# Kernel tuning notes

Hardware: AMD Instinct MI355X
Metric: run time of the kernel (lower is better)

The kernel has to match this reference:

```python
import jax, jax.numpy as jnp
import numpy as np

FEATURE_DIM = 256
TEMP = 0.1
BASE_TEMP = 0.07
MAX_SAMPLES = 1024
SIM_THR = 0.7


def setup_inputs() -> dict:
    key = jax.random.key(0)
    ks = jax.random.split(key, 8)
    B, C, H, W = 4, FEATURE_DIM, 160, 160
    s = 1.0 / np.sqrt(C)
    return {
        'feats': jax.random.normal(ks[0], (B, C, H, W), jnp.float32),
        'labels': jax.random.randint(ks[1], (B, H, W), 0, 2).astype(jnp.int64),
        'superpixel_indice': jax.random.randint(ks[2], (B, H, W), 0, 200).astype(jnp.int64),
        'w1': jax.random.normal(ks[3], (C, C), jnp.float32) * s,
        'b1': jnp.zeros((C,), jnp.float32),
        'w2': jax.random.normal(ks[4], (C, C), jnp.float32) * s,
        'b2': jnp.zeros((C,), jnp.float32),
        'wa1': jax.random.normal(ks[5], (64, C), jnp.float32) * s,
        'ba1': jnp.zeros((64,), jnp.float32),
        'wa2': jax.random.normal(ks[6], (1, 64), jnp.float32) * (1.0 / 8.0),
        'ba2': jnp.zeros((1,), jnp.float32),
    }


def _per_sample(f, w, lab, sp):
    # f: (N, C) normalized proj feats, w: (N,) pixel weights, lab/sp: (N,) int
    valid = lab == 1
    # deterministic sample: stable-sort valid pixels to the front, take MAX_SAMPLES
    order = jnp.argsort(jnp.where(valid, 0, 1).astype(jnp.int32))
    idx = order[:MAX_SAMPLES]
    sel = valid[idx]                       # (S,) real-sample mask (pads if <S valid)
    tf = f[idx]                            # (S, C)
    tw = w[idx]                            # (S,)
    ts = sp[idx]                           # (S,)
    sim = tf @ tf.T                        # (S, S)
    S = MAX_SAMPLES
    eye = jnp.eye(S, dtype=bool)
    pos = (ts[:, None] == ts[None, :]) & (sim > SIM_THR)
    pos = pos & sel[:, None] & sel[None, :] & ~eye
    exp_sim = jnp.exp(sim / TEMP) * sel[None, :].astype(sim.dtype)
    denom = exp_sim.sum(axis=1)            # (S,)
    log_prob = sim / TEMP - jnp.log(jnp.where(denom > 0, denom, 1.0))[:, None]
    pw = tw[:, None] * tw[None, :]
    pwm = jnp.where(pos, pw, 0.0)
    psum = pwm.sum()
    loss = -(TEMP / BASE_TEMP) * (pwm * jnp.where(pos, log_prob, 0.0)).sum() / jnp.where(psum > 0, psum, 1.0)
    has = psum > 0
    return jnp.where(has, loss, 0.0), has


def reference(feats, labels, superpixel_indice, w1, b1, w2, b2, wa1, ba1, wa2, ba2):
    B, C, H, W = feats.shape
    x = jnp.transpose(feats, (0, 2, 3, 1)).reshape(B, H * W, C)  # (B, N, C)
    proj = jax.nn.relu(x @ w1.T + b1) @ w2.T + b2                # 1x1 convs == per-pixel matmul
    attn = jax.nn.sigmoid(jax.nn.relu(x @ wa1.T + ba1) @ wa2.T + ba2)[..., 0]  # (B, N)
    nrm = jnp.linalg.norm(proj, axis=-1, keepdims=True)
    fn = proj / jnp.maximum(nrm, 1e-12)
    lab = labels.reshape(B, -1)
    sp = superpixel_indice.reshape(B, -1)
    losses, flags = jax.vmap(_per_sample)(fn, attn, lab, sp)
    n = flags.sum().astype(jnp.float32)
    return jnp.where(n > 0, losses.sum() / jnp.maximum(n, 1.0), 0.0)
```

## Files before the change

### kernel.cpp

```cpp
#include <hip/hip_runtime.h>
#include <hip/hip_bf16.h>
#include <math.h>

#define NPIX   25600
#define CDIM   256
#define SSEL   1024
#define BATCH  4
#define NCHUNK 25
#define INV_T  10.0f
#define RATIO  1.4285714285714286f
#define THR    0.7f

typedef __attribute__((ext_vector_type(8))) short bf16x8;
typedef __attribute__((ext_vector_type(4))) float f32x4;
typedef unsigned short u16;

__device__ __forceinline__ u16 to_bf16(float v) {
  __hip_bfloat16 h = __float2bfloat16(v);
  return *reinterpret_cast<u16*>(&h);
}

__global__ __launch_bounds__(256) void pack_weights(
    const float* __restrict__ w1, const float* __restrict__ w2,
    const float* __restrict__ wa1, const int* __restrict__ labels,
    u16* __restrict__ w1b, u16* __restrict__ w2b, u16* __restrict__ wab,
    float* __restrict__ denom, float* __restrict__ Prow, float* __restrict__ Ssum,
    int* __restrict__ counts) {
  int t = threadIdx.x;
  int e = blockIdx.x * 256 + t;
  if (e < 65536) {
    w1b[e] = to_bf16(w1[e]);
    w2b[e] = to_bf16(w2[e]);
  }
  if (e < 16384) wab[e] = to_bf16(wa1[e]);
  if (e < BATCH * SSEL) { denom[e] = 0.f; Prow[e] = 0.f; }
  if (e < BATCH) Ssum[e] = 0.f;

  if (blockIdx.x < BATCH * NCHUNK) {
    int b = blockIdx.x / NCHUNK, ch = blockIdx.x % NCHUNK;
    const int* lab = labels + b * NPIX + ch * 1024;
    int local = 0;
#pragma unroll
    for (int qq = 0; qq < 4; ++qq) local += (lab[qq * 256 + t] == 1);
    for (int off = 32; off > 0; off >>= 1) local += __shfl_xor(local, off, 64);
    __shared__ int ws[4];
    if ((t & 63) == 0) ws[t >> 6] = local;
    __syncthreads();
    if (t == 0) counts[blockIdx.x] = ws[0] + ws[1] + ws[2] + ws[3];
  }
}

__global__ __launch_bounds__(1024) void select_scatter(
    const int* __restrict__ labels, const int* __restrict__ sp,
    const int* __restrict__ counts,
    int* __restrict__ idx, int* __restrict__ selv, int* __restrict__ tsp) {
  int b = blockIdx.x / NCHUNK, ch = blockIdx.x % NCHUNK;
  int t = threadIdx.x;
  __shared__ int cs[NCHUNK];
  __shared__ int wave_tot[16];
  if (t < NCHUNK) cs[t] = counts[b * NCHUNK + t];
  __syncthreads();
  int Vtot = 0, vbase = 0;
#pragma unroll
  for (int c = 0; c < NCHUNK; ++c) {
    int v = cs[c];
    Vtot += v;
    if (c < ch) vbase += v;
  }
  int ibase = ch * 1024 - vbase;

  int i = ch * 1024 + t;
  int isv = (labels[b * NPIX + i] == 1) ? 1 : 0;
  int lane = t & 63, wid = t >> 6;
  unsigned long long mv = __ballot(isv);
  int pv = __popcll(mv & ((1ull << lane) - 1ull));
  if (lane == 0) wave_tot[wid] = __popcll(mv);
  __syncthreads();
  for (int w = 0; w < wid; ++w) pv += wave_tot[w];
  int gslot = isv ? (vbase + pv) : (Vtot + ibase + (t - pv));
  if (gslot < SSEL) {
    idx [b * SSEL + gslot] = i;
    selv[b * SSEL + gslot] = isv;
    tsp [b * SSEL + gslot] = sp[b * NPIX + i];
  }
}

__global__ __launch_bounds__(256) void gather_cast(
    const float* __restrict__ feats, const int* __restrict__ idx,
    u16* __restrict__ xh) {
  int r0 = blockIdx.x * 16;
  int b  = r0 >> 10;
  int t  = threadIdx.x;
  __shared__ int ridx[16];
  if (t < 16) ridx[t] = idx[r0 + t];
  __syncthreads();
  const float* fb = feats + ((long)b * CDIM + t) * NPIX;
#pragma unroll 4
  for (int r = 0; r < 16; ++r) {
    xh[(long)(r0 + r) * CDIM + t] = to_bf16(fb[ridx[r]]);
  }
}

__global__ __launch_bounds__(256) void gemm1_kernel(
    const u16* __restrict__ xh, const u16* __restrict__ w1b,
    const u16* __restrict__ wab,
    const float* __restrict__ b1, const float* __restrict__ ba1,
    const float* __restrict__ wa2, const float* __restrict__ ba2,
    u16* __restrict__ hh, float* __restrict__ tw) {
  int n  = blockIdx.x;
  int i0 = blockIdx.y * 64;
  int t = threadIdx.x;
  int lane = t & 63, w = t >> 6, m = lane & 15, q = lane >> 4;
  bool attn = (n == 4);
  const u16* bsrc = attn ? wab : (w1b + n * 64 * 256);

  __shared__ __align__(16) u16 Ah[64 * 72];
  __shared__ __align__(16) u16 Bh[64 * 72];

  f32x4 acc[4];
#pragma unroll
  for (int nt = 0; nt < 4; ++nt) acc[nt] = {0.f, 0.f, 0.f, 0.f};

  for (int kk = 0; kk < 4; ++kk) {
    __syncthreads();
#pragma unroll
    for (int p = 0; p < 2; ++p) {
      int e = p * 256 + t;
      int row = e >> 3, kg = e & 7;
      int lo = row * 72 + kg * 8;
      *(uint4*)&Ah[lo] = *(const uint4*)&xh[(i0 + row) * 256 + kk * 64 + kg * 8];
      *(uint4*)&Bh[lo] = *(const uint4*)&bsrc[row * 256 + kk * 64 + kg * 8];
    }
    __syncthreads();
#pragma unroll
    for (int ks = 0; ks < 2; ++ks) {
      int koff = ks * 32 + q * 8;
      bf16x8 ah = *(const bf16x8*)&Ah[(w * 16 + m) * 72 + koff];
#pragma unroll
      for (int nt = 0; nt < 4; ++nt) {
        bf16x8 bh = *(const bf16x8*)&Bh[(nt * 16 + m) * 72 + koff];
        acc[nt] = __builtin_amdgcn_mfma_f32_16x16x32_bf16(ah, bh, acc[nt], 0, 0, 0);
      }
    }
  }

  if (!attn) {
#pragma unroll
    for (int nt = 0; nt < 4; ++nt) {
      int col = n * 64 + nt * 16 + m;
      float bb = b1[col];
#pragma unroll
      for (int reg = 0; reg < 4; ++reg) {
        int row = i0 + w * 16 + q * 4 + reg;
        hh[row * 256 + col] = to_bf16(fmaxf(acc[nt][reg] + bb, 0.f));
      }
    }
  } else {
    float part[4] = {0.f, 0.f, 0.f, 0.f};
#pragma unroll
    for (int nt = 0; nt < 4; ++nt) {
      int ca = nt * 16 + m;
      float bb = ba1[ca], wv = wa2[ca];
#pragma unroll
      for (int reg = 0; reg < 4; ++reg)
        part[reg] += fmaxf(acc[nt][reg] + bb, 0.f) * wv;
    }
    for (int off = 8; off > 0; off >>= 1) {
#pragma unroll
      for (int reg = 0; reg < 4; ++reg)
        part[reg] += __shfl_xor(part[reg], off, 64);
    }
    if (m == 0) {
      float bb2 = ba2[0];
#pragma unroll
      for (int reg = 0; reg < 4; ++reg) {
        int row = i0 + w * 16 + q * 4 + reg;
        tw[row] = 1.f / (1.f + expf(-(part[reg] + bb2)));
      }
    }
  }
}

__global__ __launch_bounds__(256) void gemm2norm_kernel(
    const u16* __restrict__ hh, const u16* __restrict__ w2b,
    const float* __restrict__ b2, u16* __restrict__ fnb) {
  int i0 = blockIdx.x * 64;
  int t = threadIdx.x;
  int lane = t & 63, w = t >> 6, m = lane & 15, q = lane >> 4;

  __shared__ __align__(16) u16 Bs[64 * 264];

  bf16x8 af[8];
#pragma unroll
  for (int ks = 0; ks < 8; ++ks)
    af[ks] = *(const bf16x8*)&hh[(i0 + w * 16 + m) * 256 + ks * 32 + q * 8];

  f32x4 acc[4][4];
#pragma unroll
  for (int n = 0; n < 4; ++n)
#pragma unroll
    for (int nt = 0; nt < 4; ++nt) acc[n][nt] = {0.f, 0.f, 0.f, 0.f};

  for (int n = 0; n < 4; ++n) {
    __syncthreads();
#pragma unroll
    for (int i = 0; i < 8; ++i) {
      int e = i * 256 + t;
      int row = e >> 5, kg = e & 31;
      *(uint4*)&Bs[row * 264 + kg * 8] = *(const uint4*)&w2b[(n * 64 + row) * 256 + kg * 8];
    }
    __syncthreads();
#pragma unroll
    for (int ks = 0; ks < 8; ++ks) {
      int koff = ks * 32 + q * 8;
#pragma unroll
      for (int nt = 0; nt < 4; ++nt) {
        bf16x8 bh = *(const bf16x8*)&Bs[(nt * 16 + m) * 264 + koff];
        acc[n][nt] = __builtin_amdgcn_mfma_f32_16x16x32_bf16(af[ks], bh, acc[n][nt], 0, 0, 0);
      }
    }
  }

  float ss[4] = {0.f, 0.f, 0.f, 0.f};
#pragma unroll
  for (int n = 0; n < 4; ++n)
#pragma unroll
    for (int nt = 0; nt < 4; ++nt) {
      float bb = b2[n * 64 + nt * 16 + m];
#pragma unroll
      for (int reg = 0; reg < 4; ++reg) {
        float p = acc[n][nt][reg] + bb;
        acc[n][nt][reg] = p;
        ss[reg] += p * p;
      }
    }
  for (int off = 8; off > 0; off >>= 1) {
#pragma unroll
    for (int reg = 0; reg < 4; ++reg) ss[reg] += __shfl_xor(ss[reg], off, 64);
  }
  float inv[4];
#pragma unroll
  for (int reg = 0; reg < 4; ++reg)
    inv[reg] = 1.f / fmaxf(sqrtf(ss[reg]), 1e-12f);

#pragma unroll
  for (int n = 0; n < 4; ++n)
#pragma unroll
    for (int nt = 0; nt < 4; ++nt) {
      int col = n * 64 + nt * 16 + m;
#pragma unroll
      for (int reg = 0; reg < 4; ++reg) {
        int row = i0 + w * 16 + q * 4 + reg;
        fnb[row * 256 + col] = to_bf16(acc[n][nt][reg] * inv[reg]);
      }
    }
}

__global__ __launch_bounds__(256) void sim_kernel(
    const u16* __restrict__ fnb, const float* __restrict__ tw,
    const int* __restrict__ selv, const int* __restrict__ tsp,
    float* __restrict__ denom, float* __restrict__ Prow, float* __restrict__ Ssum) {
  int b = blockIdx.y;
  int t = threadIdx.x;
  int lane = t & 63, w = t >> 6;
  int m = lane & 15, q = lane >> 4;

  int rem = blockIdx.x, ti = 0;
  while (rem >= (16 - ti)) { rem -= (16 - ti); ++ti; }
  int tj = ti + rem;
  bool diag = (ti == tj);
  int i0 = ti * 64, j0 = tj * 64;
  int base = b << 10;

  __shared__ __align__(16) u16 Ah[64 * 72];
  __shared__ __align__(16) u16 Bhh[64 * 72];
  __shared__ float drl[64], Prl[64];
  __shared__ float dclw[4][64], Pclw[4][64];
  __shared__ float swv[4];

  const u16* Bh = diag ? Ah : Bhh;

  f32x4 acc[4];
#pragma unroll
  for (int nt = 0; nt < 4; ++nt) acc[nt] = {0.f, 0.f, 0.f, 0.f};

  for (int kk = 0; kk < 4; ++kk) {
    __syncthreads();
#pragma unroll
    for (int p = 0; p < 2; ++p) {
      int e = p * 256 + t;
      int row = e >> 3, kg = e & 7;
      int lo = row * 72 + kg * 8;
      *(uint4*)&Ah[lo] = *(const uint4*)&fnb[(base + i0 + row) * 256 + kk * 64 + kg * 8];
      if (!diag)
        *(uint4*)&Bhh[lo] = *(const uint4*)&fnb[(base + j0 + row) * 256 + kk * 64 + kg * 8];
    }
    __syncthreads();
#pragma unroll
    for (int ks = 0; ks < 2; ++ks) {
      int koff = ks * 32 + q * 8;
      bf16x8 ah = *(const bf16x8*)&Ah[(w * 16 + m) * 72 + koff];
#pragma unroll
      for (int nt = 0; nt < 4; ++nt) {
        bf16x8 bh = *(const bf16x8*)&Bh[(nt * 16 + m) * 72 + koff];
        acc[nt] = __builtin_amdgcn_mfma_f32_16x16x32_bf16(ah, bh, acc[nt], 0, 0, 0);
      }
    }
  }

  int   gi[4], gj[4], si[4], sj[4], ci[4], cj[4];
  float twi[4], twj[4];
#pragma unroll
  for (int reg = 0; reg < 4; ++reg) {
    int i = i0 + w * 16 + q * 4 + reg;
    gi[reg] = i; twi[reg] = tw[base + i];
    si[reg] = selv[base + i]; ci[reg] = tsp[base + i];
  }
#pragma unroll
  for (int nt = 0; nt < 4; ++nt) {
    int j = j0 + nt * 16 + m;
    gj[nt] = j; twj[nt] = tw[base + j];
    sj[nt] = selv[base + j]; cj[nt] = tsp[base + j];
  }

  float dR[4] = {0, 0, 0, 0}, PR[4] = {0, 0, 0, 0};
  float dC[4] = {0, 0, 0, 0}, PC[4] = {0, 0, 0, 0};
  float Sp = 0.f;
#pragma unroll
  for (int nt = 0; nt < 4; ++nt) {
#pragma unroll
    for (int reg = 0; reg < 4; ++reg) {
      float s = acc[nt][reg];
      float e10 = __expf(s * INV_T);
      if (sj[nt]) dR[reg] += e10;
      if (si[reg]) dC[nt] += e10;
      if (si[reg] && sj[nt] && (ci[reg] == cj[nt]) && (s > THR) && (gi[reg] != gj[nt])) {
        float pw = twi[reg] * twj[nt];
        PR[reg] += pw;
        PC[nt] += pw;
        Sp += pw * s;
      }
    }
  }

  for (int off = 8; off > 0; off >>= 1) {
#pragma unroll
    for (int reg = 0; reg < 4; ++reg) {
      dR[reg] += __shfl_xor(dR[reg], off, 64);
      PR[reg] += __shfl_xor(PR[reg], off, 64);
    }
  }
  if (m == 0) {
#pragma unroll
    for (int reg = 0; reg < 4; ++reg) {
      drl[w * 16 + q * 4 + reg] = dR[reg];
      Prl[w * 16 + q * 4 + reg] = PR[reg];
    }
  }
  if (!diag) {
    for (int off = 32; off >= 16; off >>= 1) {
#pragma unroll
      for (int nt = 0; nt < 4; ++nt) {
        dC[nt] += __shfl_xor(dC[nt], off, 64);
        PC[nt] += __shfl_xor(PC[nt], off, 64);
      }
    }
    if (q == 0) {
#pragma unroll
      for (int nt = 0; nt < 4; ++nt) {
        dclw[w][nt * 16 + m] = dC[nt];
        Pclw[w][nt * 16 + m] = PC[nt];
      }
    }
  }
  for (int off = 32; off > 0; off >>= 1) Sp += __shfl_xor(Sp, off, 64);
  if (lane == 0) swv[w] = Sp;
  __syncthreads();

  if (t < 64) {
    atomicAdd(&denom[base + i0 + t], drl[t]);
    atomicAdd(&Prow [base + i0 + t], Prl[t]);
    if (!diag) {
      float dc = dclw[0][t] + dclw[1][t] + dclw[2][t] + dclw[3][t];
      float pc = Pclw[0][t] + Pclw[1][t] + Pclw[2][t] + Pclw[3][t];
      atomicAdd(&denom[base + j0 + t], dc);
      atomicAdd(&Prow [base + j0 + t], pc);
    }
  }
  if (t == 0) {
    float St = swv[0] + swv[1] + swv[2] + swv[3];
    atomicAdd(&Ssum[b], diag ? St : 2.f * St);
  }
}

__global__ __launch_bounds__(1024) void finalize_kernel(
    const float* __restrict__ denom, const float* __restrict__ Prow,
    const float* __restrict__ Ssum, float* __restrict__ out) {
  int t = threadIdx.x;
  int b = t >> 8, u = t & 255;
  float P = 0.f, L = 0.f;
#pragma unroll
  for (int q = 0; q < 4; ++q) {
    int s = u + q * 256;
    float p = Prow[b * SSEL + s];
    float D = denom[b * SSEL + s];
    P += p;
    L += p * logf(D > 0.f ? D : 1.f);
  }
  for (int off = 32; off > 0; off >>= 1) {
    P += __shfl_xor(P, off, 64);
    L += __shfl_xor(L, off, 64);
  }
  __shared__ float wP[16], wL[16];
  int lane = t & 63, w = t >> 6;
  if (lane == 0) { wP[w] = P; wL[w] = L; }
  __syncthreads();
  if (t == 0) {
    float total = 0.f, n = 0.f;
    for (int bb = 0; bb < BATCH; ++bb) {
      float psum = wP[4 * bb] + wP[4 * bb + 1] + wP[4 * bb + 2] + wP[4 * bb + 3];
      float lsum = wL[4 * bb] + wL[4 * bb + 1] + wL[4 * bb + 2] + wL[4 * bb + 3];
      if (psum > 0.f) {
        float wls = Ssum[bb] * INV_T - lsum;
        total += -RATIO * wls / psum;
        n += 1.f;
      }
    }
    out[0] = (n > 0.f) ? (total / n) : 0.f;
  }
}

extern "C" void kernel_launch(void* const* d_in, const int* in_sizes, int n_in,
                              void* d_out, int out_size, void* d_ws, size_t ws_size,
                              hipStream_t stream) {
  const float* feats = (const float*)d_in[0];
  const int*   labels = (const int*)d_in[1];
  const int*   sp     = (const int*)d_in[2];
  const float* w1  = (const float*)d_in[3];
  const float* b1  = (const float*)d_in[4];
  const float* w2  = (const float*)d_in[5];
  const float* b2  = (const float*)d_in[6];
  const float* wa1 = (const float*)d_in[7];
  const float* ba1 = (const float*)d_in[8];
  const float* wa2 = (const float*)d_in[9];
  const float* ba2 = (const float*)d_in[10];
  float* out = (float*)d_out;

  char* W = (char*)d_ws;
  u16* w1b = (u16*)W;               W += 65536 * 2;
  u16* w2b = (u16*)W;               W += 65536 * 2;
  u16* wab = (u16*)W;               W += 16384 * 2;
  u16* xh  = (u16*)W;               W += 1048576 * 2;
  u16* hh  = (u16*)W;               W += 1048576 * 2;
  u16* fnb = (u16*)W;               W += 1048576 * 2;
  float* tw   = (float*)W;          W += 4096 * 4;
  float* denom= (float*)W;          W += 4096 * 4;
  float* Prow = (float*)W;          W += 4096 * 4;
  float* Ssum = (float*)W;          W += 4 * 4;
  int*   idx  = (int*)W;            W += 4096 * 4;
  int*   selv = (int*)W;            W += 4096 * 4;
  int*   tsp  = (int*)W;            W += 4096 * 4;
  int*   counts = (int*)W;          W += 128 * 4;

  pack_weights<<<256, 256, 0, stream>>>(w1, w2, wa1, labels, w1b, w2b, wab,
                                        denom, Prow, Ssum, counts);
  select_scatter<<<BATCH * NCHUNK, 1024, 0, stream>>>(labels, sp, counts,
                                                      idx, selv, tsp);
  gather_cast<<<256, 256, 0, stream>>>(feats, idx, xh);
  gemm1_kernel<<<dim3(5, 64), 256, 0, stream>>>(xh, w1b, wab, b1, ba1,
                                                wa2, ba2, hh, tw);
  gemm2norm_kernel<<<64, 256, 0, stream>>>(hh, w2b, b2, fnb);
  sim_kernel<<<dim3(136, BATCH), 256, 0, stream>>>(fnb, tw, selv, tsp,
                                                   denom, Prow, Ssum);
  finalize_kernel<<<1, 1024, 0, stream>>>(denom, Prow, Ssum, out);
}
```

Before: 197.1 us.

## Fuse pipeline into three kernels: merged prep, fused MLP, sim with last-block finalize

Merges label counting and scatter into one prep kernel, where each block recounts all chunks itself, and folds the weight casts into extra blocks of it. Fuses the gather, first GEMM, attention head, second GEMM and normalisation into one kernel, keeping intermediates in shared memory and reading weights straight from global memory. Finalize moves into the sim kernel through a last-block atomic counter, and the sim tile is loaded in one pass with full K. This cuts seven launches to three and removes the xh/hh round trips through global memory, but the fused MLP runs only 64 blocks and each prep block reads labels 25 times.

```diff
diff --git a/kernel.cpp b/kernel.cpp
--- a/kernel.cpp
+++ b/kernel.cpp
@@ -10,6 +10,7 @@
 #define INV_T  10.0f
 #define RATIO  1.4285714285714286f
 #define THR    0.7f
+#define NBLK_SIM (136 * BATCH)
 
 typedef __attribute__((ext_vector_type(8))) short bf16x8;
 typedef __attribute__((ext_vector_type(4))) float f32x4;
@@ -20,238 +21,202 @@
   return *reinterpret_cast<u16*>(&h);
 }
 
-__global__ __launch_bounds__(256) void pack_weights(
+__global__ __launch_bounds__(1024) void prep_kernel(
     const float* __restrict__ w1, const float* __restrict__ w2,
-    const float* __restrict__ wa1, const int* __restrict__ labels,
+    const float* __restrict__ wa1,
+    const int* __restrict__ labels, const int* __restrict__ sp,
     u16* __restrict__ w1b, u16* __restrict__ w2b, u16* __restrict__ wab,
-    float* __restrict__ denom, float* __restrict__ Prow, float* __restrict__ Ssum,
-    int* __restrict__ counts) {
+    float* __restrict__ denom, float* __restrict__ Prow,
+    float* __restrict__ Ssum, unsigned* __restrict__ donecnt,
+    int* __restrict__ idx, int* __restrict__ selv, int* __restrict__ tsp) {
+  __shared__ int wcnt[NCHUNK][16];
+  __shared__ int cs[NCHUNK];
   int t = threadIdx.x;
-  int e = blockIdx.x * 256 + t;
-  if (e < 65536) {
+  int blk = blockIdx.x;
+
+  if (blk < BATCH * NCHUNK) {
+    int b = blk / NCHUNK, ch = blk % NCHUNK;
+    int lane = t & 63, wid = t >> 6;
+    int my_isv = 0;
+    unsigned long long my_mv = 0;
+    for (int c = 0; c < NCHUNK; ++c) {
+      int isv = (labels[b * NPIX + c * 1024 + t] == 1) ? 1 : 0;
+      unsigned long long mv = __ballot(isv);
+      if (c == ch) { my_isv = isv; my_mv = mv; }
+      if (lane == 0) wcnt[c][wid] = __popcll(mv);
+    }
+    __syncthreads();
+    if (t < NCHUNK) {
+      int s = 0;
+      for (int w = 0; w < 16; ++w) s += wcnt[t][w];
+      cs[t] = s;
+    }
+    __syncthreads();
+    int Vtot = 0, vbase = 0;
+    for (int c = 0; c < NCHUNK; ++c) {
+      int v = cs[c];
+      Vtot += v;
+      if (c < ch) vbase += v;
+    }
+    int ibase = ch * 1024 - vbase;
+    int pv = __popcll(my_mv & ((1ull << lane) - 1ull));
+    for (int w = 0; w < wid; ++w) pv += wcnt[ch][w];
+    int i = ch * 1024 + t;
+    int gslot = my_isv ? (vbase + pv) : (Vtot + ibase + (t - pv));
+    if (gslot < SSEL) {
+      idx [b * SSEL + gslot] = i;
+      selv[b * SSEL + gslot] = my_isv;
+      tsp [b * SSEL + gslot] = sp[b * NPIX + i];
+    }
+  } else {
+    int e = (blk - BATCH * NCHUNK) * 1024 + t;
     w1b[e] = to_bf16(w1[e]);
     w2b[e] = to_bf16(w2[e]);
-  }
-  if (e < 16384) wab[e] = to_bf16(wa1[e]);
-  if (e < BATCH * SSEL) { denom[e] = 0.f; Prow[e] = 0.f; }
-  if (e < BATCH) Ssum[e] = 0.f;
-
-  if (blockIdx.x < BATCH * NCHUNK) {
-    int b = blockIdx.x / NCHUNK, ch = blockIdx.x % NCHUNK;
-    const int* lab = labels + b * NPIX + ch * 1024;
-    int local = 0;
-#pragma unroll
-    for (int qq = 0; qq < 4; ++qq) local += (lab[qq * 256 + t] == 1);
-    for (int off = 32; off > 0; off >>= 1) local += __shfl_xor(local, off, 64);
-    __shared__ int ws[4];
-    if ((t & 63) == 0) ws[t >> 6] = local;
-    __syncthreads();
-    if (t == 0) counts[blockIdx.x] = ws[0] + ws[1] + ws[2] + ws[3];
+    if (e < 16384) wab[e] = to_bf16(wa1[e]);
+    if (e < BATCH * SSEL) { denom[e] = 0.f; Prow[e] = 0.f; }
+    if (e < BATCH) Ssum[e] = 0.f;
+    if (e == 0) *donecnt = 0u;
   }
 }
 
-__global__ __launch_bounds__(1024) void select_scatter(
-    const int* __restrict__ labels, const int* __restrict__ sp,
-    const int* __restrict__ counts,
-    int* __restrict__ idx, int* __restrict__ selv, int* __restrict__ tsp) {
-  int b = blockIdx.x / NCHUNK, ch = blockIdx.x % NCHUNK;
-  int t = threadIdx.x;
-  __shared__ int cs[NCHUNK];
-  __shared__ int wave_tot[16];
-  if (t < NCHUNK) cs[t] = counts[b * NCHUNK + t];
-  __syncthreads();
-  int Vtot = 0, vbase = 0;
-#pragma unroll
-  for (int c = 0; c < NCHUNK; ++c) {
-    int v = cs[c];
-    Vtot += v;
-    if (c < ch) vbase += v;
-  }
-  int ibase = ch * 1024 - vbase;
-
-  int i = ch * 1024 + t;
-  int isv = (labels[b * NPIX + i] == 1) ? 1 : 0;
-  int lane = t & 63, wid = t >> 6;
-  unsigned long long mv = __ballot(isv);
-  int pv = __popcll(mv & ((1ull << lane) - 1ull));
-  if (lane == 0) wave_tot[wid] = __popcll(mv);
-  __syncthreads();
-  for (int w = 0; w < wid; ++w) pv += wave_tot[w];
-  int gslot = isv ? (vbase + pv) : (Vtot + ibase + (t - pv));
-  if (gslot < SSEL) {
-    idx [b * SSEL + gslot] = i;
-    selv[b * SSEL + gslot] = isv;
-    tsp [b * SSEL + gslot] = sp[b * NPIX + i];
-  }
-}
-
-__global__ __launch_bounds__(256) void gather_cast(
+__global__ __launch_bounds__(256) void mlp_fused(
     const float* __restrict__ feats, const int* __restrict__ idx,
-    u16* __restrict__ xh) {
-  int r0 = blockIdx.x * 16;
-  int b  = r0 >> 10;
-  int t  = threadIdx.x;
-  __shared__ int ridx[16];
-  if (t < 16) ridx[t] = idx[r0 + t];
-  __syncthreads();
-  const float* fb = feats + ((long)b * CDIM + t) * NPIX;
-#pragma unroll 4
-  for (int r = 0; r < 16; ++r) {
-    xh[(long)(r0 + r) * CDIM + t] = to_bf16(fb[ridx[r]]);
-  }
-}
-
-__global__ __launch_bounds__(256) void gemm1_kernel(
-    const u16* __restrict__ xh, const u16* __restrict__ w1b,
+    const u16* __restrict__ w1b, const u16* __restrict__ w2b,
     const u16* __restrict__ wab,
     const float* __restrict__ b1, const float* __restrict__ ba1,
     const float* __restrict__ wa2, const float* __restrict__ ba2,
-    u16* __restrict__ hh, float* __restrict__ tw) {
-  int n  = blockIdx.x;
-  int i0 = blockIdx.y * 64;
-  int t = threadIdx.x;
+    const float* __restrict__ b2,
+    u16* __restrict__ fnb, float* __restrict__ tw) {
+  int i0 = blockIdx.x * 64;
+  int b  = i0 >> 10;
+  int t  = threadIdx.x;
   int lane = t & 63, w = t >> 6, m = lane & 15, q = lane >> 4;
-  bool attn = (n == 4);
-  const u16* bsrc = attn ? wab : (w1b + n * 64 * 256);
-
-  __shared__ __align__(16) u16 Ah[64 * 72];
-  __shared__ __align__(16) u16 Bh[64 * 72];
-
-  f32x4 acc[4];
-#pragma unroll
-  for (int nt = 0; nt < 4; ++nt) acc[nt] = {0.f, 0.f, 0.f, 0.f};
-
-  for (int kk = 0; kk < 4; ++kk) {
-    __syncthreads();
-#pragma unroll
-    for (int p = 0; p < 2; ++p) {
-      int e = p * 256 + t;
-      int row = e >> 3, kg = e & 7;
-      int lo = row * 72 + kg * 8;
-      *(uint4*)&Ah[lo] = *(const uint4*)&xh[(i0 + row) * 256 + kk * 64 + kg * 8];
-      *(uint4*)&Bh[lo] = *(const uint4*)&bsrc[row * 256 + kk * 64 + kg * 8];
-    }
-    __syncthreads();
-#pragma unroll
-    for (int ks = 0; ks < 2; ++ks) {
+
+  __shared__ __align__(16) u16 xs[64 * 264];
+  __shared__ __align__(16) u16 hs[64 * 264];
+  __shared__ int ridx[64];
+
+  if (t < 64) ridx[t] = idx[i0 + t];
+  __syncthreads();
+
+  const float* fb = feats + ((long)b * CDIM + t) * NPIX;
+#pragma unroll 8
+  for (int r = 0; r < 64; ++r)
+    xs[r * 264 + t] = to_bf16(fb[ridx[r]]);
+  __syncthreads();
+
+  bf16x8 af[8];
+#pragma unroll
+  for (int ks = 0; ks < 8; ++ks)
+    af[ks] = *(const bf16x8*)&xs[(w * 16 + m) * 264 + ks * 32 + q * 8];
+
+  for (int g = 0; g < 5; ++g) {
+    bool attn = (g == 4);
+    const u16* bsrc = attn ? wab : (w1b + g * 64 * 256);
+    f32x4 acc[4];
+#pragma unroll
+    for (int nt = 0; nt < 4; ++nt) acc[nt] = {0.f, 0.f, 0.f, 0.f};
+#pragma unroll
+    for (int ks = 0; ks < 8; ++ks) {
       int koff = ks * 32 + q * 8;
-      bf16x8 ah = *(const bf16x8*)&Ah[(w * 16 + m) * 72 + koff];
-#pragma unroll
-      for (int nt = 0; nt < 4; ++nt) {
-        bf16x8 bh = *(const bf16x8*)&Bh[(nt * 16 + m) * 72 + koff];
-        acc[nt] = __builtin_amdgcn_mfma_f32_16x16x32_bf16(ah, bh, acc[nt], 0, 0, 0);
-      }
-    }
-  }
-
-  if (!attn) {
+#pragma unroll
+      for (int nt = 0; nt < 4; ++nt) {
+        bf16x8 bh = *(const bf16x8*)&bsrc[(nt * 16 + m) * 256 + koff];
+        acc[nt] = __builtin_amdgcn_mfma_f32_16x16x32_bf16(af[ks], bh, acc[nt], 0, 0, 0);
+      }
+    }
+    if (!attn) {
+#pragma unroll
+      for (int nt = 0; nt < 4; ++nt) {
+        int col = g * 64 + nt * 16 + m;
+        float bb = b1[col];
+#pragma unroll
+        for (int reg = 0; reg < 4; ++reg)
+          hs[(w * 16 + q * 4 + reg) * 264 + col] =
+              to_bf16(fmaxf(acc[nt][reg] + bb, 0.f));
+      }
+    } else {
+      float part[4] = {0.f, 0.f, 0.f, 0.f};
+#pragma unroll
+      for (int nt = 0; nt < 4; ++nt) {
+        int ca = nt * 16 + m;
+        float bb = ba1[ca], wv = wa2[ca];
+#pragma unroll
+        for (int reg = 0; reg < 4; ++reg)
+          part[reg] += fmaxf(acc[nt][reg] + bb, 0.f) * wv;
+      }
+      for (int off = 8; off > 0; off >>= 1) {
+#pragma unroll
+        for (int reg = 0; reg < 4; ++reg)
+          part[reg] += __shfl_xor(part[reg], off, 64);
+      }
+      if (m == 0) {
+        float bb2 = ba2[0];
+#pragma unroll
+        for (int reg = 0; reg < 4; ++reg) {
+          int row = i0 + w * 16 + q * 4 + reg;
+          tw[row] = 1.f / (1.f + expf(-(part[reg] + bb2)));
+        }
+      }
+    }
+  }
+  __syncthreads();
+
+  bf16x8 hf[8];
+#pragma unroll
+  for (int ks = 0; ks < 8; ++ks)
+    hf[ks] = *(const bf16x8*)&hs[(w * 16 + m) * 264 + ks * 32 + q * 8];
+
+  f32x4 acc2[4][4];
+#pragma unroll
+  for (int n = 0; n < 4; ++n)
+#pragma unroll
+    for (int nt = 0; nt < 4; ++nt) acc2[n][nt] = {0.f, 0.f, 0.f, 0.f};
+
+#pragma unroll
+  for (int n = 0; n < 4; ++n) {
+#pragma unroll
+    for (int ks = 0; ks < 8; ++ks) {
+      int koff = ks * 32 + q * 8;
+#pragma unroll
+      for (int nt = 0; nt < 4; ++nt) {
+        bf16x8 bh = *(const bf16x8*)&w2b[(n * 64 + nt * 16 + m) * 256 + koff];
+        acc2[n][nt] = __builtin_amdgcn_mfma_f32_16x16x32_bf16(hf[ks], bh, acc2[n][nt], 0, 0, 0);
+      }
+    }
+  }
+
+  float ss[4] = {0.f, 0.f, 0.f, 0.f};
+#pragma unroll
+  for (int n = 0; n < 4; ++n)
+#pragma unroll
+    for (int nt = 0; nt < 4; ++nt) {
+      float bb = b2[n * 64 + nt * 16 + m];
+#pragma unroll
+      for (int reg = 0; reg < 4; ++reg) {
+        float p = acc2[n][nt][reg] + bb;
+        acc2[n][nt][reg] = p;
+        ss[reg] += p * p;
+      }
+    }
+  for (int off = 8; off > 0; off >>= 1) {
+#pragma unroll
+    for (int reg = 0; reg < 4; ++reg) ss[reg] += __shfl_xor(ss[reg], off, 64);
+  }
+  float inv[4];
+#pragma unroll
+  for (int reg = 0; reg < 4; ++reg)
+    inv[reg] = 1.f / fmaxf(sqrtf(ss[reg]), 1e-12f);
+
+#pragma unroll
+  for (int n = 0; n < 4; ++n)
 #pragma unroll
     for (int nt = 0; nt < 4; ++nt) {
       int col = n * 64 + nt * 16 + m;
-      float bb = b1[col];
 #pragma unroll
       for (int reg = 0; reg < 4; ++reg) {
         int row = i0 + w * 16 + q * 4 + reg;
-        hh[row * 256 + col] = to_bf16(fmaxf(acc[nt][reg] + bb, 0.f));
-      }
-    }
-  } else {
-    float part[4] = {0.f, 0.f, 0.f, 0.f};
-#pragma unroll
-    for (int nt = 0; nt < 4; ++nt) {
-      int ca = nt * 16 + m;
-      float bb = ba1[ca], wv = wa2[ca];
-#pragma unroll
-      for (int reg = 0; reg < 4; ++reg)
-        part[reg] += fmaxf(acc[nt][reg] + bb, 0.f) * wv;
-    }
-    for (int off = 8; off > 0; off >>= 1) {
-#pragma unroll
-      for (int reg = 0; reg < 4; ++reg)
-        part[reg] += __shfl_xor(part[reg], off, 64);
-    }
-    if (m == 0) {
-      float bb2 = ba2[0];
-#pragma unroll
-      for (int reg = 0; reg < 4; ++reg) {
-        int row = i0 + w * 16 + q * 4 + reg;
-        tw[row] = 1.f / (1.f + expf(-(part[reg] + bb2)));
-      }
-    }
-  }
-}
-
-__global__ __launch_bounds__(256) void gemm2norm_kernel(
-    const u16* __restrict__ hh, const u16* __restrict__ w2b,
-    const float* __restrict__ b2, u16* __restrict__ fnb) {
-  int i0 = blockIdx.x * 64;
-  int t = threadIdx.x;
-  int lane = t & 63, w = t >> 6, m = lane & 15, q = lane >> 4;
-
-  __shared__ __align__(16) u16 Bs[64 * 264];
-
-  bf16x8 af[8];
-#pragma unroll
-  for (int ks = 0; ks < 8; ++ks)
-    af[ks] = *(const bf16x8*)&hh[(i0 + w * 16 + m) * 256 + ks * 32 + q * 8];
-
-  f32x4 acc[4][4];
-#pragma unroll
-  for (int n = 0; n < 4; ++n)
-#pragma unroll
-    for (int nt = 0; nt < 4; ++nt) acc[n][nt] = {0.f, 0.f, 0.f, 0.f};
-
-  for (int n = 0; n < 4; ++n) {
-    __syncthreads();
-#pragma unroll
-    for (int i = 0; i < 8; ++i) {
-      int e = i * 256 + t;
-      int row = e >> 5, kg = e & 31;
-      *(uint4*)&Bs[row * 264 + kg * 8] = *(const uint4*)&w2b[(n * 64 + row) * 256 + kg * 8];
-    }
-    __syncthreads();
-#pragma unroll
-    for (int ks = 0; ks < 8; ++ks) {
-      int koff = ks * 32 + q * 8;
-#pragma unroll
-      for (int nt = 0; nt < 4; ++nt) {
-        bf16x8 bh = *(const bf16x8*)&Bs[(nt * 16 + m) * 264 + koff];
-        acc[n][nt] = __builtin_amdgcn_mfma_f32_16x16x32_bf16(af[ks], bh, acc[n][nt], 0, 0, 0);
-      }
-    }
-  }
-
-  float ss[4] = {0.f, 0.f, 0.f, 0.f};
-#pragma unroll
-  for (int n = 0; n < 4; ++n)
-#pragma unroll
-    for (int nt = 0; nt < 4; ++nt) {
-      float bb = b2[n * 64 + nt * 16 + m];
-#pragma unroll
-      for (int reg = 0; reg < 4; ++reg) {
-        float p = acc[n][nt][reg] + bb;
-        acc[n][nt][reg] = p;
-        ss[reg] += p * p;
-      }
-    }
-  for (int off = 8; off > 0; off >>= 1) {
-#pragma unroll
-    for (int reg = 0; reg < 4; ++reg) ss[reg] += __shfl_xor(ss[reg], off, 64);
-  }
-  float inv[4];
-#pragma unroll
-  for (int reg = 0; reg < 4; ++reg)
-    inv[reg] = 1.f / fmaxf(sqrtf(ss[reg]), 1e-12f);
-
-#pragma unroll
-  for (int n = 0; n < 4; ++n)
-#pragma unroll
-    for (int nt = 0; nt < 4; ++nt) {
-      int col = n * 64 + nt * 16 + m;
-#pragma unroll
-      for (int reg = 0; reg < 4; ++reg) {
-        int row = i0 + w * 16 + q * 4 + reg;
-        fnb[row * 256 + col] = to_bf16(acc[n][nt][reg] * inv[reg]);
+        fnb[row * 256 + col] = to_bf16(acc2[n][nt][reg] * inv[reg]);
       }
     }
 }
@@ -259,7 +224,9 @@
 __global__ __launch_bounds__(256) void sim_kernel(
     const u16* __restrict__ fnb, const float* __restrict__ tw,
     const int* __restrict__ selv, const int* __restrict__ tsp,
-    float* __restrict__ denom, float* __restrict__ Prow, float* __restrict__ Ssum) {
+    float* __restrict__ denom, float* __restrict__ Prow,
+    float* __restrict__ Ssum, unsigned* __restrict__ donecnt,
+    float* __restrict__ out) {
   int b = blockIdx.y;
   int t = threadIdx.x;
   int lane = t & 63, w = t >> 6;
@@ -272,39 +239,39 @@
   int i0 = ti * 64, j0 = tj * 64;
   int base = b << 10;
 
-  __shared__ __align__(16) u16 Ah[64 * 72];
-  __shared__ __align__(16) u16 Bhh[64 * 72];
+  __shared__ __align__(16) u16 Ah[64 * 264];
+  __shared__ __align__(16) u16 Bhh[64 * 264];
   __shared__ float drl[64], Prl[64];
   __shared__ float dclw[4][64], Pclw[4][64];
   __shared__ float swv[4];
+  __shared__ unsigned lastv;
+  __shared__ float wPf[4][4], wLf[4][4];
 
   const u16* Bh = diag ? Ah : Bhh;
 
+#pragma unroll
+  for (int p = 0; p < 8; ++p) {
+    int e = p * 256 + t;
+    int row = e >> 5, kg = e & 31;
+    *(uint4*)&Ah[row * 264 + kg * 8] =
+        *(const uint4*)&fnb[(base + i0 + row) * 256 + kg * 8];
+    if (!diag)
+      *(uint4*)&Bhh[row * 264 + kg * 8] =
+          *(const uint4*)&fnb[(base + j0 + row) * 256 + kg * 8];
+  }
+  __syncthreads();
+
   f32x4 acc[4];
 #pragma unroll
   for (int nt = 0; nt < 4; ++nt) acc[nt] = {0.f, 0.f, 0.f, 0.f};
-
-  for (int kk = 0; kk < 4; ++kk) {
-    __syncthreads();
-#pragma unroll
-    for (int p = 0; p < 2; ++p) {
-      int e = p * 256 + t;
-      int row = e >> 3, kg = e & 7;
-      int lo = row * 72 + kg * 8;
-      *(uint4*)&Ah[lo] = *(const uint4*)&fnb[(base + i0 + row) * 256 + kk * 64 + kg * 8];
-      if (!diag)
-        *(uint4*)&Bhh[lo] = *(const uint4*)&fnb[(base + j0 + row) * 256 + kk * 64 + kg * 8];
-    }
-    __syncthreads();
-#pragma unroll
-    for (int ks = 0; ks < 2; ++ks) {
-      int koff = ks * 32 + q * 8;
-      bf16x8 ah = *(const bf16x8*)&Ah[(w * 16 + m) * 72 + koff];
-#pragma unroll
-      for (int nt = 0; nt < 4; ++nt) {
-        bf16x8 bh = *(const bf16x8*)&Bh[(nt * 16 + m) * 72 + koff];
-        acc[nt] = __builtin_amdgcn_mfma_f32_16x16x32_bf16(ah, bh, acc[nt], 0, 0, 0);
-      }
+#pragma unroll
+  for (int ks = 0; ks < 8; ++ks) {
+    int koff = ks * 32 + q * 8;
+    bf16x8 ah = *(const bf16x8*)&Ah[(w * 16 + m) * 264 + koff];
+#pragma unroll
+    for (int nt = 0; nt < 4; ++nt) {
+      bf16x8 bh = *(const bf16x8*)&Bh[(nt * 16 + m) * 264 + koff];
+      acc[nt] = __builtin_amdgcn_mfma_f32_16x16x32_bf16(ah, bh, acc[nt], 0, 0, 0);
     }
   }
 
@@ -391,37 +358,44 @@
     float St = swv[0] + swv[1] + swv[2] + swv[3];
     atomicAdd(&Ssum[b], diag ? St : 2.f * St);
   }
-}
-
-__global__ __launch_bounds__(1024) void finalize_kernel(
-    const float* __restrict__ denom, const float* __restrict__ Prow,
-    const float* __restrict__ Ssum, float* __restrict__ out) {
-  int t = threadIdx.x;
-  int b = t >> 8, u = t & 255;
-  float P = 0.f, L = 0.f;
-#pragma unroll
-  for (int q = 0; q < 4; ++q) {
-    int s = u + q * 256;
-    float p = Prow[b * SSEL + s];
-    float D = denom[b * SSEL + s];
-    P += p;
-    L += p * logf(D > 0.f ? D : 1.f);
+
+  __threadfence();
+  if (t == 0)
+    lastv = __hip_atomic_fetch_add(donecnt, 1u, __ATOMIC_ACQ_REL,
+                                   __HIP_MEMORY_SCOPE_AGENT);
+  __syncthreads();
+  if (lastv != NBLK_SIM - 1) return;
+
+  float Pb[4] = {0.f, 0.f, 0.f, 0.f}, Lb[4] = {0.f, 0.f, 0.f, 0.f};
+#pragma unroll
+  for (int k = 0; k < 16; ++k) {
+    int bb = k >> 2;
+    int s = bb * SSEL + (k & 3) * 256 + t;
+    float p = __hip_atomic_load(&Prow[s], __ATOMIC_RELAXED, __HIP_MEMORY_SCOPE_AGENT);
+    float D = __hip_atomic_load(&denom[s], __ATOMIC_RELAXED, __HIP_MEMORY_SCOPE_AGENT);
+    Pb[bb] += p;
+    Lb[bb] += p * logf(D > 0.f ? D : 1.f);
   }
   for (int off = 32; off > 0; off >>= 1) {
-    P += __shfl_xor(P, off, 64);
-    L += __shfl_xor(L, off, 64);
-  }
-  __shared__ float wP[16], wL[16];
-  int lane = t & 63, w = t >> 6;
-  if (lane == 0) { wP[w] = P; wL[w] = L; }
+#pragma unroll
+    for (int bb = 0; bb < 4; ++bb) {
+      Pb[bb] += __shfl_xor(Pb[bb], off, 64);
+      Lb[bb] += __shfl_xor(Lb[bb], off, 64);
+    }
+  }
+  if (lane == 0) {
+#pragma unroll
+    for (int bb = 0; bb < 4; ++bb) { wPf[w][bb] = Pb[bb]; wLf[w][bb] = Lb[bb]; }
+  }
   __syncthreads();
   if (t == 0) {
     float total = 0.f, n = 0.f;
     for (int bb = 0; bb < BATCH; ++bb) {
-      float psum = wP[4 * bb] + wP[4 * bb + 1] + wP[4 * bb + 2] + wP[4 * bb + 3];
-      float lsum = wL[4 * bb] + wL[4 * bb + 1] + wL[4 * bb + 2] + wL[4 * bb + 3];
+      float psum = wPf[0][bb] + wPf[1][bb] + wPf[2][bb] + wPf[3][bb];
+      float lsum = wLf[0][bb] + wLf[1][bb] + wLf[2][bb] + wLf[3][bb];
+      float Sb = __hip_atomic_load(&Ssum[bb], __ATOMIC_RELAXED, __HIP_MEMORY_SCOPE_AGENT);
       if (psum > 0.f) {
-        float wls = Ssum[bb] * INV_T - lsum;
+        float wls = Sb * INV_T - lsum;
         total += -RATIO * wls / psum;
         n += 1.f;
       }
@@ -450,8 +424,6 @@
   u16* w1b = (u16*)W;               W += 65536 * 2;
   u16* w2b = (u16*)W;               W += 65536 * 2;
   u16* wab = (u16*)W;               W += 16384 * 2;
-  u16* xh  = (u16*)W;               W += 1048576 * 2;
-  u16* hh  = (u16*)W;               W += 1048576 * 2;
   u16* fnb = (u16*)W;               W += 1048576 * 2;
   float* tw   = (float*)W;          W += 4096 * 4;
   float* denom= (float*)W;          W += 4096 * 4;
@@ -460,17 +432,13 @@
   int*   idx  = (int*)W;            W += 4096 * 4;
   int*   selv = (int*)W;            W += 4096 * 4;
   int*   tsp  = (int*)W;            W += 4096 * 4;
-  int*   counts = (int*)W;          W += 128 * 4;
-
-  pack_weights<<<256, 256, 0, stream>>>(w1, w2, wa1, labels, w1b, w2b, wab,
-                                        denom, Prow, Ssum, counts);
-  select_scatter<<<BATCH * NCHUNK, 1024, 0, stream>>>(labels, sp, counts,
-                                                      idx, selv, tsp);
-  gather_cast<<<256, 256, 0, stream>>>(feats, idx, xh);
-  gemm1_kernel<<<dim3(5, 64), 256, 0, stream>>>(xh, w1b, wab, b1, ba1,
-                                                wa2, ba2, hh, tw);
-  gemm2norm_kernel<<<64, 256, 0, stream>>>(hh, w2b, b2, fnb);
-  sim_kernel<<<dim3(136, BATCH), 256, 0, stream>>>(fnb, tw, selv, tsp,
-                                                   denom, Prow, Ssum);
-  finalize_kernel<<<1, 1024, 0, stream>>>(denom, Prow, Ssum, out);
+  unsigned* donecnt = (unsigned*)W; W += 4;
+
+  prep_kernel<<<BATCH * NCHUNK + 64, 1024, 0, stream>>>(
+      w1, w2, wa1, labels, sp, w1b, w2b, wab,
+      denom, Prow, Ssum, donecnt, idx, selv, tsp);
+  mlp_fused<<<64, 256, 0, stream>>>(feats, idx, w1b, w2b, wab,
+                                    b1, ba1, wa2, ba2, b2, fnb, tw);
+  sim_kernel<<<dim3(136, BATCH), 256, 0, stream>>>(
+      fnb, tw, selv, tsp, denom, Prow, Ssum, donecnt, out);
 }
```

After: 263.4 us. 1.34x slower.
